# Kernel optimization log

Hardware: AMD Instinct MI355X
Metric: run time of the kernel (lower is better)

The kernel has to match this reference:

```python
import jax, jax.numpy as jnp
import numpy as np

P = 8          # patch_size
EPS = 1e-6     # LayerNorm2d eps


def _conv(x, w, b, groups=1):
    # x: (B,Cin,H,W), w: (Cout, Cin//groups, kh, kw)
    y = jax.lax.conv_general_dilated(
        x, w, window_strides=(1, 1), padding='SAME',
        feature_group_count=groups,
        dimension_numbers=('NCHW', 'OIHW', 'NCHW'))
    return y + b[None, :, None, None]


def _ln2d(x, w, b):
    mu = jnp.mean(x, axis=1, keepdims=True)
    var = jnp.mean((x - mu) ** 2, axis=1, keepdims=True)
    y = (x - mu) / jnp.sqrt(var + EPS)
    return w[None, :, None, None] * y + b[None, :, None, None]


def _fft_mix(x, fw):
    # windowed rFFT2 -> per-(channel,freq) real weight -> irFFT2.
    # H,W divisible by P, so window_partitionx == plain window partition.
    B, C, H, W = x.shape
    nh, nw = H // P, W // P
    xw = x.reshape(B, C, nh, P, nw, P).transpose(0, 2, 4, 1, 3, 5)  # (B,nh,nw,C,P,P)
    f = jnp.fft.rfft2(xw)                    # (B,nh,nw,C,P,P//2+1)
    f = f * fw                               # fw: (C,P,P//2+1) broadcasts
    xw = jnp.fft.irfft2(f, s=(P, P))
    return xw.transpose(0, 3, 1, 4, 2, 5).reshape(B, C, H, W)


def _gelu(x):
    return jax.nn.gelu(x, approximate=False)  # torch nn.GELU default = exact erf


def setup_inputs() -> dict:
    key = jax.random.key(0)
    ks = jax.random.split(key, 18)
    B, C, H, W = 4, 64, 256, 256
    C4, D = C * 4, C // 4
    f32 = jnp.float32

    def n(k, shape, s):
        return (jax.random.normal(k, shape, f32) * s)

    return {
        'x': jax.random.normal(ks[0], (B, C, H, W), f32),
        'ln_w': jnp.ones((C,), f32),
        'ln_b': jnp.zeros((C,), f32),
        'pconv_w': n(ks[1], (D, D, 3, 3), 0.08),
        'pconv_b': n(ks[2], (D,), 0.02),
        'w0': n(ks[3], (C4, C, 1, 1), 0.12),
        'b0': n(ks[4], (C4,), 0.02),
        'w1': n(ks[5], (C4, C, 1, 1), 0.12),
        'b1': n(ks[6], (C4,), 0.02),
        'w2': n(ks[7], (C, C4, 1, 1), 0.06),
        'b2': n(ks[8], (C,), 0.02),
        'w3': n(ks[9], (C4, 1, 3, 3), 0.3),
        'b3': n(ks[10], (C4,), 0.02),
        'w4': n(ks[11], (C, C4, 1, 1), 0.06),
        'b4': n(ks[12], (C,), 0.02),
        'fftw1': 1.0 + n(ks[13], (C, P, P // 2 + 1), 0.1),
        'fftw2': 1.0 + n(ks[14], (C, P, P // 2 + 1), 0.1),
    }


def reference(x, ln_w, ln_b, pconv_w, pconv_b, w0, b0, w1, b1,
              w2, b2, w3, b3, w4, b4, fftw1, fftw2):
    C = x.shape[1]
    D = C // 4
    C4 = C * 4

    xn = _ln2d(x, ln_w, ln_b)

    # partial 3x3 conv on first C//4 channels
    y1 = _conv(xn[:, :D], pconv_w, pconv_b)
    x2 = jnp.concatenate([y1, xn[:, D:]], axis=1)

    # branch 1: 1x1 expand -> GELU -> 1x1 contract -> windowed FFT mixing
    x1 = _conv(xn, w0, b0)
    x1 = _gelu(x1)
    x1 = _conv(x1, w2, b2)
    x1 = _fft_mix(x1, fftw1)

    # branch 2: 1x1 expand -> GELU -> depthwise 3x3 -> GELU -> 1x1 contract -> FFT mixing
    x2 = _conv(x2, w1, b1)
    x2 = _gelu(x2)
    x2 = _conv(x2, w3, b3, groups=C4)
    x2 = _gelu(x2)
    x2 = _conv(x2, w4, b4)
    x2 = _fft_mix(x2, fftw2)

    return x1 + x2
```

## Files before the change

### kernel.cpp

```cpp
#include <hip/hip_runtime.h>


typedef _Float16 f16;
typedef _Float16 f16x2 __attribute__((ext_vector_type(2)));
typedef _Float16 f16x4 __attribute__((ext_vector_type(4)));
typedef _Float16 f16x8 __attribute__((ext_vector_type(8)));
typedef float f32x4 __attribute__((ext_vector_type(4)));

__device__ __forceinline__ float dot2f(f16x2 a, f16x2 b, float c) {
#if __has_builtin(__builtin_amdgcn_fdot2)
  return __builtin_amdgcn_fdot2(a, b, c, false);
#else
  return c + (float)a.x * (float)b.x + (float)a.y * (float)b.y;
#endif
}

__device__ __forceinline__ f16x2 gelu_pk(f16x2 x) {
  const f16x2 c1 = {(f16)1.5957691f, (f16)1.5957691f};
  const f16x2 c3 = {(f16)0.0713548f, (f16)0.0713548f};
  const f16x2 cl = {(f16)-1.4426950f, (f16)-1.4426950f};
  f16x2 x2 = x * x;
  f16x2 u = x * (c1 + c3 * x2);
  f16x2 a = cl * u;
  f16 t0, t1;
#if __has_builtin(__builtin_amdgcn_exp2h)
  t0 = __builtin_amdgcn_exp2h(a[0]);
  t1 = __builtin_amdgcn_exp2h(a[1]);
#else
  t0 = (f16)exp2f((float)a[0]);
  t1 = (f16)exp2f((float)a[1]);
#endif
  f16 d0 = (f16)1.0f + t0, d1 = (f16)1.0f + t1;
  f16 r0, r1;
#if __has_builtin(__builtin_amdgcn_rcph)
  r0 = __builtin_amdgcn_rcph(d0);
  r1 = __builtin_amdgcn_rcph(d1);
#else
  r0 = (f16)(1.0f / (float)d0);
  r1 = (f16)(1.0f / (float)d1);
#endif
  f16x2 r = {r0, r1};
  return x * r;
}

__device__ __forceinline__ f16x2 cvtpk(float a, float b) {
  return __builtin_bit_cast(f16x2, __builtin_amdgcn_cvt_pkrtz(a, b));
}

__global__ void __launch_bounds__(256) lnpre_kernel(
    const float* __restrict__ x, const float* __restrict__ lnw,
    const float* __restrict__ lnb, f16* __restrict__ xn,
    const float* __restrict__ w0, const float* __restrict__ w1,
    const float* __restrict__ w2, const float* __restrict__ w4,
    const float* __restrict__ w3, const float* __restrict__ b3,
    const float* __restrict__ fw1, const float* __restrict__ fw2,
    f16* __restrict__ W0h, f16* __restrict__ W1h,
    f16* __restrict__ W2h, f16* __restrict__ W4h,
    f16* __restrict__ w3pk, f16* __restrict__ b3pk,
    float* __restrict__ kap1, float* __restrict__ kap2) {
  __shared__ float Wt[4][64];
  __shared__ float ct[8];
  int blk = blockIdx.x, t = threadIdx.x;
  if (blk < 1024) {
    int b = blk >> 8;
    int px = (blk & 255) * 256 + t;
    const float* xp = x + ((size_t)b << 22) + px;
    float v[64];
    float s = 0.f;
#pragma unroll
    for (int c = 0; c < 64; ++c) { v[c] = xp[(size_t)c << 16]; s += v[c]; }
    float mu = s * (1.f / 64.f), s2 = 0.f;
#pragma unroll
    for (int c = 0; c < 64; ++c) { float d = v[c] - mu; s2 += d * d; }
    float rstd = rsqrtf(s2 * (1.f / 64.f) + 1e-6f);
    f16* op = xn + (size_t)b * 4194304 + (size_t)px * 64;
#pragma unroll
    for (int g = 0; g < 8; ++g) {
      f16x8 pk;
#pragma unroll
      for (int j = 0; j < 8; ++j) {
        int c = g * 8 + j;
        pk[j] = (f16)((v[c] - mu) * rstd * lnw[c] + lnb[c]);
      }
      *(f16x8*)(op + g * 8) = pk;
    }
    return;
  }
  if (blk < 1290) {
    int i = (blk - 1024) * 256 + t;
    if (i < 16384) W0h[i] = (f16)w0[i];
    else if (i < 32768) W1h[i - 16384] = (f16)w1[i - 16384];
    else if (i < 49152) W2h[i - 32768] = (f16)w2[i - 32768];
    else if (i < 65536) W4h[i - 49152] = (f16)w4[i - 49152];
    else if (i < 67840) {
      int j = i - 65536;
      int g = j / 72, r = j % 72, tap = r >> 3, k = r & 7;
      w3pk[j] = (f16)w3[(g * 8 + k) * 9 + tap];
    } else if (i < 68096) {
      int k = i - 67840;
      b3pk[k] = (f16)b3[k];
    }
    return;
  }
  int sub = t >> 6, lane = t & 63;
  int unit = (blk - 1290) * 4 + sub;
  int which = unit >> 6, c = unit & 63;
  const float* fw = which ? fw2 : fw1;
  float* kap = which ? kap2 : kap1;
  int a = lane >> 3, bb = lane & 7;
  if (t == 0) {
    const float r2 = 0.70710678118654752440f;
    ct[0] = 1.f; ct[1] = r2; ct[2] = 0.f; ct[3] = -r2;
    ct[4] = -1.f; ct[5] = -r2; ct[6] = 0.f; ct[7] = r2;
  }
  Wt[sub][lane] = (bb <= 4) ? fw[c * 40 + a * 5 + bb]
                            : fw[c * 40 + ((8 - a) & 7) * 5 + (8 - bb)];
  __syncthreads();
  float acc = 0.f;
  for (int u = 0; u < 8; ++u)
    for (int v = 0; v < 8; ++v)
      acc += Wt[sub][u * 8 + v] * ct[(u * a + v * bb) & 7];
  kap[c * 64 + lane] = acc * 0.015625f;
}

__device__ __forceinline__ void pconv_body(
    char* smem, int blk, int b, const f16* __restrict__ xn,
    const float* __restrict__ pw, const float* __restrict__ pb,
    f16* __restrict__ y1) {
  char* halo = smem;
  f16* wpk = (f16*)(smem + 11520);
  float* pbs = (float*)(smem + 16128);
  int t = threadIdx.x;
  const f16* xnb = xn + (size_t)b * 4194304;
  f16* y1b = y1 + (size_t)b * 1048576;
  int h0 = (blk >> 4) << 4, w0 = (blk & 15) << 4;
  for (int i = t; i < 2304; i += 256) {
    int co = i / 144, r = i % 144, tap = r >> 4, ci = r & 15;
    wpk[i] = (f16)pw[co * 144 + ci * 9 + tap];
  }
  if (t < 16) pbs[t] = pb[t];
  for (int i = 0; i < 3; ++i) {
    int u = i * 256 + t;
    if (u < 648) {
      int hp = u >> 1, half = u & 1;
      int hr = hp / 18, hc = hp - hr * 18;
      int h = h0 - 1 + hr, w = w0 - 1 + hc;
      f16x8 v = {0, 0, 0, 0, 0, 0, 0, 0};
      if ((unsigned)h < 256u && (unsigned)w < 256u)
        v = *(const f16x8*)(xnb + ((((size_t)h << 8)) + w) * 64 + half * 8);
      *(f16x8*)(halo + hr * 640 + ((hc * 32 + half * 16) ^ ((hr & 7) << 4))) = v;
    }
  }
  __syncthreads();
  int rl = t >> 4, cl = t & 15;
  float acc[16];
#pragma unroll
  for (int co = 0; co < 16; ++co) acc[co] = pbs[co];
#pragma unroll
  for (int ty = 0; ty < 3; ++ty)
#pragma unroll
    for (int tx = 0; tx < 3; ++tx) {
      int hr = rl + ty, hc = cl + tx, tap = ty * 3 + tx;
      f16x8 ld0 = *(const f16x8*)(halo + hr * 640 + ((hc * 32) ^ ((hr & 7) << 4)));
      f16x8 ld1 = *(const f16x8*)(halo + hr * 640 + ((hc * 32 + 16) ^ ((hr & 7) << 4)));
#pragma unroll
      for (int co = 0; co < 16; ++co) {
#pragma unroll
        for (int p = 0; p < 4; ++p) {
          f16x2 xp = {ld0[2 * p], ld0[2 * p + 1]};
          f16x2 wp = *(const f16x2*)&wpk[co * 144 + tap * 16 + 2 * p];
          acc[co] = dot2f(xp, wp, acc[co]);
        }
#pragma unroll
        for (int p = 0; p < 4; ++p) {
          f16x2 xp = {ld1[2 * p], ld1[2 * p + 1]};
          f16x2 wp = *(const f16x2*)&wpk[co * 144 + tap * 16 + 8 + 2 * p];
          acc[co] = dot2f(xp, wp, acc[co]);
        }
      }
    }
  size_t px = (((size_t)(h0 + rl)) << 8) + w0 + cl;
  f16x8 o0, o1;
#pragma unroll
  for (int j = 0; j < 8; ++j) { o0[j] = (f16)acc[j]; o1[j] = (f16)acc[8 + j]; }
  *(f16x8*)(y1b + px * 16) = o0;
  *(f16x8*)(y1b + px * 16 + 8) = o1;
}

__device__ __forceinline__ void b1_body(
    char* smem, int sub, int b, const f16* __restrict__ xn,
    const f16* __restrict__ W0h, const float* __restrict__ b0,
    const f16* __restrict__ W2h, const float* __restrict__ b2,
    f16* __restrict__ u1d, f16* __restrict__ u1w) {
  f16* Es = (f16*)smem;
  int t = threadIdx.x;
  const f16* xnb = xn + (size_t)b * 4194304;
  f16* u1b = (b < 3) ? (u1d + (size_t)b * 4194304) : u1w;
  int px0 = sub << 7;
  int l = t & 63, wv = t >> 6, lm = l & 15, kg = l >> 4;
  f16x8 a[2][2];
#pragma unroll
  for (int mt = 0; mt < 2; ++mt) {
    int row = wv * 32 + mt * 16 + lm;
#pragma unroll
    for (int kk = 0; kk < 2; ++kk)
      a[mt][kk] = *(const f16x8*)(xnb + (size_t)(px0 + row) * 64 + kk * 32 + kg * 8);
  }
  f32x4 uacc[2][4];
#pragma unroll
  for (int aa = 0; aa < 2; ++aa)
#pragma unroll
    for (int n = 0; n < 4; ++n) uacc[aa][n] = (f32x4){0.f, 0.f, 0.f, 0.f};
  for (int cc = 0; cc < 4; ++cc) {
    f32x4 eacc[2][4];
#pragma unroll
    for (int aa = 0; aa < 2; ++aa)
#pragma unroll
      for (int n = 0; n < 4; ++n) eacc[aa][n] = (f32x4){0.f, 0.f, 0.f, 0.f};
#pragma unroll
    for (int kk = 0; kk < 2; ++kk) {
      f16x8 bf[4];
#pragma unroll
      for (int nt = 0; nt < 4; ++nt) {
        int co = cc * 64 + nt * 16 + lm;
        bf[nt] = *(const f16x8*)(W0h + (size_t)co * 64 + kk * 32 + kg * 8);
      }
#pragma unroll
      for (int mt = 0; mt < 2; ++mt)
#pragma unroll
        for (int nt = 0; nt < 4; ++nt)
          eacc[mt][nt] = __builtin_amdgcn_mfma_f32_16x16x32_f16(bf[nt], a[mt][kk], eacc[mt][nt], 0, 0, 0);
    }
    if (cc) __syncthreads();
#pragma unroll
    for (int mt = 0; mt < 2; ++mt) {
      int row = wv * 32 + mt * 16 + lm;
#pragma unroll
      for (int nt = 0; nt < 4; ++nt) {
        int c0 = nt * 16 + kg * 4;
        float4 bz4 = *(const float4*)&b0[cc * 64 + c0];
        f16x2 lo = gelu_pk(cvtpk(eacc[mt][nt][0] + bz4.x, eacc[mt][nt][1] + bz4.y));
        f16x2 hi = gelu_pk(cvtpk(eacc[mt][nt][2] + bz4.z, eacc[mt][nt][3] + bz4.w));
        f16x4 pk = {lo[0], lo[1], hi[0], hi[1]};
        *(f16x4*)((char*)Es + row * 128 + ((c0 * 2) ^ ((row & 7) << 4))) = pk;
      }
    }
    __syncthreads();
#pragma unroll
    for (int kk = 0; kk < 2; ++kk) {
      int kb = kk * 64 + kg * 16;
      f16x8 af[2];
#pragma unroll
      for (int mt = 0; mt < 2; ++mt) {
        int row = wv * 32 + mt * 16 + lm;
        af[mt] = *(const f16x8*)((char*)Es + row * 128 + (kb ^ ((row & 7) << 4)));
      }
      f16x8 bf[4];
#pragma unroll
      for (int nt = 0; nt < 4; ++nt) {
        int co = nt * 16 + lm;
        bf[nt] = *(const f16x8*)(W2h + (size_t)co * 256 + cc * 64 + kk * 32 + kg * 8);
      }
#pragma unroll
      for (int mt = 0; mt < 2; ++mt)
#pragma unroll
        for (int nt = 0; nt < 4; ++nt)
          uacc[mt][nt] = __builtin_amdgcn_mfma_f32_16x16x32_f16(bf[nt], af[mt], uacc[mt][nt], 0, 0, 0);
    }
    __syncthreads();
  }
#pragma unroll
  for (int mt = 0; mt < 2; ++mt) {
    int row = wv * 32 + mt * 16 + lm;
#pragma unroll
    for (int nt = 0; nt < 4; ++nt) {
      int c0 = nt * 16 + kg * 4;
      float4 bz4 = *(const float4*)&b2[c0];
      f16x2 lo = cvtpk(uacc[mt][nt][0] + bz4.x, uacc[mt][nt][1] + bz4.y);
      f16x2 hi = cvtpk(uacc[mt][nt][2] + bz4.z, uacc[mt][nt][3] + bz4.w);
      f16x4 pk = {lo[0], lo[1], hi[0], hi[1]};
      *(f16x4*)((char*)Es + row * 128 + ((c0 * 2) ^ ((row & 7) << 4))) = pk;
    }
  }
  __syncthreads();
  int co = t >> 2, q = t & 3;
  f16x8 o[4];
#pragma unroll
  for (int i = 0; i < 32; ++i) {
    int m = q * 32 + i;
    o[i >> 3][i & 7] =
        *(const f16*)((char*)Es + m * 128 + ((co * 2) ^ ((m & 7) << 4)));
  }
  f16* up = u1b + ((size_t)co << 16) + px0 + q * 32;
#pragma unroll
  for (int ss = 0; ss < 4; ++ss) *(f16x8*)(up + ss * 8) = o[ss];
}

__global__ void __launch_bounds__(256) b1pc_kernel(
    const f16* __restrict__ xn, const f16* __restrict__ W0h,
    const float* __restrict__ b0, const f16* __restrict__ W2h,
    const float* __restrict__ b2, f16* __restrict__ u1d,
    f16* __restrict__ u1w, const float* __restrict__ pw,
    const float* __restrict__ pb, f16* __restrict__ y1) {
  __shared__ __align__(16) char smem[16384];
  int xb = blockIdx.x;
  if (xb < 2048)
    b1_body(smem, xb & 511, xb >> 9, xn, W0h, b0, W2h, b2, u1d, u1w);
  else {
    int u = xb - 2048;
    pconv_body(smem, u & 255, u >> 8, xn, pw, pb, y1);
  }
}

__device__ __forceinline__ void b2_expand(
    const f16x8 (&a0)[3], const f16x8 (&a1)[3], const f16* __restrict__ W1h,
    int ce0, int lm, int kg, f32x4 (&eacc)[3][2]) {
#pragma unroll
  for (int a = 0; a < 3; ++a)
#pragma unroll
    for (int n = 0; n < 2; ++n) eacc[a][n] = (f32x4){0.f, 0.f, 0.f, 0.f};
#pragma unroll
  for (int kk = 0; kk < 2; ++kk) {
    f16x8 bf[2];
#pragma unroll
    for (int nt = 0; nt < 2; ++nt) {
      int ce = ce0 + nt * 16 + lm;
      bf[nt] = *(const f16x8*)(W1h + (size_t)ce * 64 + kk * 32 + kg * 8);
    }
#pragma unroll
    for (int mtl = 0; mtl < 3; ++mtl) {
      f16x8 af = kk ? a1[mtl] : a0[mtl];
#pragma unroll
      for (int nt = 0; nt < 2; ++nt)
        eacc[mtl][nt] = __builtin_amdgcn_mfma_f32_16x16x32_f16(bf[nt], af, eacc[mtl][nt], 0, 0, 0);
    }
  }
}

__global__ void __launch_bounds__(256) b2_kernel(
    const f16* __restrict__ xn, const f16* __restrict__ y1,
    const f16* __restrict__ W1h, const float* __restrict__ b1v,
    const f16* __restrict__ W4h, const float* __restrict__ b4,
    const f16* __restrict__ w3pk, const f16* __restrict__ b3pk,
    f16* __restrict__ u2) {
  __shared__ __align__(16) f16 Es[6144];
  int t = threadIdx.x, blk = blockIdx.x, b = blockIdx.y;
  const f16* xnb = xn + (size_t)b * 4194304;
  const f16* y1b = y1 + (size_t)b * 1048576;
  f16* u2b = u2 + (size_t)b * 4194304;
  int h0 = (blk >> 4) << 3, w0 = (blk & 15) << 4;
  int l = t & 63, wv = t >> 6, lm = l & 15, kg = l >> 4;
  f16x8 a0[3], a1[3];
#pragma unroll
  for (int mtl = 0; mtl < 3; ++mtl) {
    int row = (mtl * 4 + wv) * 16 + lm;
    f16x8 v0 = {0, 0, 0, 0, 0, 0, 0, 0}, v1 = v0;
    if (row < 180) {
      int hr = row / 18, hc = row - hr * 18;
      int h = h0 - 1 + hr, w = w0 - 1 + hc;
      if ((unsigned)h < 256u && (unsigned)w < 256u) {
        size_t px = ((size_t)h << 8) + w;
        v1 = *(const f16x8*)(xnb + px * 64 + 32 + kg * 8);
        v0 = (kg < 2) ? *(const f16x8*)(y1b + px * 16 + kg * 8)
                      : *(const f16x8*)(xnb + px * 64 + kg * 8);
      }
    }
    a0[mtl] = v0;
    a1[mtl] = v1;
  }
  f32x4 uacc[2][4];
#pragma unroll
  for (int a = 0; a < 2; ++a)
#pragma unroll
    for (int n = 0; n < 4; ++n) uacc[a][n] = (f32x4){0.f, 0.f, 0.f, 0.f};
  f32x4 eacc[3][2];
  b2_expand(a0, a1, W1h, 0, lm, kg, eacc);
  for (int it = 0; it < 8; ++it) {
    int ce0 = it * 32;
    if (it) __syncthreads();
#pragma unroll
    for (int mtl = 0; mtl < 3; ++mtl) {
      int row = (mtl * 4 + wv) * 16 + lm;
#pragma unroll
      for (int nt = 0; nt < 2; ++nt) {
        int cL = nt * 16 + kg * 4;
        float4 bz4 = *(const float4*)&b1v[ce0 + cL];
        f16x2 lo = gelu_pk(cvtpk(eacc[mtl][nt][0] + bz4.x, eacc[mtl][nt][1] + bz4.y));
        f16x2 hi = gelu_pk(cvtpk(eacc[mtl][nt][2] + bz4.z, eacc[mtl][nt][3] + bz4.w));
        f16x4 pk = {lo[0], lo[1], hi[0], hi[1]};
        *(f16x4*)((char*)Es + row * 64 + ((cL * 2) ^ (((row >> 1) & 3) << 4))) = pk;
      }
    }
    __syncthreads();
    if (it < 7) b2_expand(a0, a1, W1h, ce0 + 32, lm, kg, eacc);
    int g9 = (ce0 + kg * 8) >> 3;
    f16x8 wv9[9];
#pragma unroll
    for (int tap = 0; tap < 9; ++tap)
      wv9[tap] = *(const f16x8*)(w3pk + g9 * 72 + tap * 8);
    f16x8 bias8 = *(const f16x8*)(b3pk + ce0 + kg * 8);
    f16x8 af2[2];
#pragma unroll
    for (int mt = 0; mt < 2; ++mt) {
      int px = wv * 32 + mt * 16 + lm;
      int rl2 = px >> 4, cl2 = px & 15;
      f16x8 a8 = bias8;
#pragma unroll
      for (int ty = 0; ty < 3; ++ty)
#pragma unroll
        for (int tx = 0; tx < 3; ++tx) {
          int hp = (rl2 + ty) * 18 + (cl2 + tx);
          f16x8 xv = *(const f16x8*)((char*)Es + hp * 64 + ((kg * 16) ^ (((hp >> 1) & 3) << 4)));
          a8 += xv * wv9[ty * 3 + tx];
        }
#pragma unroll
      for (int j2 = 0; j2 < 4; ++j2) {
        f16x2 g = gelu_pk((f16x2){a8[2 * j2], a8[2 * j2 + 1]});
        af2[mt][2 * j2] = g[0];
        af2[mt][2 * j2 + 1] = g[1];
      }
    }
    f16x8 bf2[4];
#pragma unroll
    for (int nt = 0; nt < 4; ++nt) {
      int co = nt * 16 + lm;
      bf2[nt] = *(const f16x8*)(W4h + (size_t)co * 256 + ce0 + kg * 8);
    }
#pragma unroll
    for (int mt = 0; mt < 2; ++mt)
#pragma unroll
      for (int nt = 0; nt < 4; ++nt)
        uacc[mt][nt] = __builtin_amdgcn_mfma_f32_16x16x32_f16(bf2[nt], af2[mt], uacc[mt][nt], 0, 0, 0);
  }
  __syncthreads();
#pragma unroll
  for (int mt = 0; mt < 2; ++mt) {
    if (mt) __syncthreads();
    int crow = wv * 16 + lm;
#pragma unroll
    for (int nt = 0; nt < 4; ++nt) {
      int c0 = nt * 16 + kg * 4;
      float4 bz4 = *(const float4*)&b4[c0];
      f16x2 lo = cvtpk(uacc[mt][nt][0] + bz4.x, uacc[mt][nt][1] + bz4.y);
      f16x2 hi = cvtpk(uacc[mt][nt][2] + bz4.z, uacc[mt][nt][3] + bz4.w);
      f16x4 pk = {lo[0], lo[1], hi[0], hi[1]};
      *(f16x4*)((char*)Es + crow * 128 + ((c0 * 2) ^ ((crow & 7) << 4))) = pk;
    }
    __syncthreads();
    int co = t >> 2, q = t & 3;
    f16x8 o0, o1;
#pragma unroll
    for (int i = 0; i < 16; ++i) {
      int crow = q * 16 + i;
      f16 vv = *(const f16*)((char*)Es + crow * 128 + ((co * 2) ^ ((crow & 7) << 4)));
      if (i < 8) o0[i] = vv;
      else o1[i - 8] = vv;
    }
    f16* up = u2b + ((size_t)co << 16) + (size_t)(h0 + 2 * q + mt) * 256 + w0;
    *(f16x8*)(up) = o0;
    *(f16x8*)(up + 8) = o1;
  }
}

__global__ void __launch_bounds__(256) fftmix_kernel(
    const f16* __restrict__ u1d, const f16* __restrict__ u1w,
    const f16* __restrict__ u2, const float* __restrict__ kap1,
    const float* __restrict__ kap2, float* __restrict__ out, int base) {
  int blk = blockIdx.x;
  int b = base + blockIdx.y;
  int c = blk >> 4, part = blk & 15;
  int t = threadIdx.x;
  int l = t & 63, wv = (t >> 6) & 3;
  int s = l >> 3, tq = l & 7;
  __shared__ unsigned int kls[64];
  if (t < 64) {
    f16 k1 = (f16)kap1[(c << 6) + t];
    f16 k2 = (f16)kap2[(c << 6) + t];
    kls[t] = (unsigned int)__builtin_bit_cast(unsigned short, k1) |
             ((unsigned int)__builtin_bit_cast(unsigned short, k2) << 16);
  }
  __syncthreads();
  unsigned int kp[64];
#pragma unroll
  for (int j = 0; j < 64; ++j) {
    int idx = (((s - (j >> 3)) & 7) << 3) | ((tq - (j & 7)) & 7);
    kp[j] = kls[idx];
  }
  const f16* u1 = (b < 3) ? (u1d + (size_t)b * 4194304) : u1w;
  const f16* u2b = u2 + (size_t)b * 4194304;
  size_t cb = ((size_t)c) << 16;
  size_t obase = ((size_t)(b * 64 + c)) << 16;
  int win0 = part * 64 + wv * 16;
  for (int it = 0; it < 16; ++it) {
    int win = win0 + it;
    int wh = win >> 5, ww = win & 31;
    size_t pix = (size_t)((wh * 8 + s) << 8) + ww * 8 + tq;
    unsigned int pk =
        (unsigned int)__builtin_bit_cast(unsigned short, u1[cb + pix]) |
        ((unsigned int)__builtin_bit_cast(unsigned short, u2b[cb + pix]) << 16);
    float ac0 = 0.f, ac1 = 0.f, ac2 = 0.f, ac3 = 0.f;
#pragma unroll
    for (int j = 0; j < 64; j += 4) {
      unsigned int v0 = (unsigned int)__builtin_amdgcn_readlane((int)pk, j);
      unsigned int v1 = (unsigned int)__builtin_amdgcn_readlane((int)pk, j + 1);
      unsigned int v2 = (unsigned int)__builtin_amdgcn_readlane((int)pk, j + 2);
      unsigned int v3 = (unsigned int)__builtin_amdgcn_readlane((int)pk, j + 3);
      ac0 = dot2f(__builtin_bit_cast(f16x2, v0), __builtin_bit_cast(f16x2, kp[j]), ac0);
      ac1 = dot2f(__builtin_bit_cast(f16x2, v1), __builtin_bit_cast(f16x2, kp[j + 1]), ac1);
      ac2 = dot2f(__builtin_bit_cast(f16x2, v2), __builtin_bit_cast(f16x2, kp[j + 2]), ac2);
      ac3 = dot2f(__builtin_bit_cast(f16x2, v3), __builtin_bit_cast(f16x2, kp[j + 3]), ac3);
    }
    out[obase + pix] = (ac0 + ac1) + (ac2 + ac3);
  }
}

__global__ void diag_kernel(float* __restrict__ out, float code, int n) {
  int i = blockIdx.x * 256 + threadIdx.x;
  for (int p = i; p < n; p += 256 * 4096) out[p] = (p == 0) ? code : 0.f;
}

extern "C" void kernel_launch(void* const* d_in, const int* in_sizes, int n_in,
                              void* d_out, int out_size, void* d_ws,
                              size_t ws_size, hipStream_t stream) {
  const float* x       = (const float*)d_in[0];
  const float* ln_w    = (const float*)d_in[1];
  const float* ln_b    = (const float*)d_in[2];
  const float* pconv_w = (const float*)d_in[3];
  const float* pconv_b = (const float*)d_in[4];
  const float* w0      = (const float*)d_in[5];
  const float* b0      = (const float*)d_in[6];
  const float* w1      = (const float*)d_in[7];
  const float* b1      = (const float*)d_in[8];
  const float* w2      = (const float*)d_in[9];
  const float* b2      = (const float*)d_in[10];
  const float* w3      = (const float*)d_in[11];
  const float* b3      = (const float*)d_in[12];
  const float* w4      = (const float*)d_in[13];
  const float* b4      = (const float*)d_in[14];
  const float* fftw1   = (const float*)d_in[15];
  const float* fftw2   = (const float*)d_in[16];

  const size_t OFF_KAP1 = 0;
  const size_t OFF_KAP2 = 16384;
  const size_t OFF_W0H  = 32768;
  const size_t OFF_W1H  = 65536;
  const size_t OFF_W2H  = 98304;
  const size_t OFF_W4H  = 131072;
  const size_t OFF_W3PK = 163840;
  const size_t OFF_B3PK = 168448;
  const size_t OFF_Y1   = 168960;
  const size_t OFF_U2   = OFF_Y1 + 8388608ull;
  const size_t OFF_U13  = OFF_U2 + 33554432ull;
  const size_t WS_NEED  = OFF_U13 + 8388608ull;

  float* outF = (float*)d_out;
  if (ws_size < WS_NEED) {
    diag_kernel<<<4096, 256, 0, stream>>>(outF, 1000.0f + (float)(ws_size >> 20), 16777216);
    return;
  }
  char* ws = (char*)d_ws;
  float* kap1 = (float*)(ws + OFF_KAP1);
  float* kap2 = (float*)(ws + OFF_KAP2);
  f16* W0h  = (f16*)(ws + OFF_W0H);
  f16* W1h  = (f16*)(ws + OFF_W1H);
  f16* W2h  = (f16*)(ws + OFF_W2H);
  f16* W4h  = (f16*)(ws + OFF_W4H);
  f16* w3pk = (f16*)(ws + OFF_W3PK);
  f16* b3pk = (f16*)(ws + OFF_B3PK);
  f16* Y1   = (f16*)(ws + OFF_Y1);
  f16* U2   = (f16*)(ws + OFF_U2);
  f16* U13  = (f16*)(ws + OFF_U13);

  f16* XN  = (f16*)d_out;
  f16* U1D = (f16*)d_out + 16777216;

  lnpre_kernel<<<1322, 256, 0, stream>>>(x, ln_w, ln_b, XN,
                                         w0, w1, w2, w4, w3, b3, fftw1, fftw2,
                                         W0h, W1h, W2h, W4h, w3pk, b3pk,
                                         kap1, kap2);
  b1pc_kernel<<<3072, 256, 0, stream>>>(XN, W0h, b0, W2h, b2, U1D, U13,
                                        pconv_w, pconv_b, Y1);
  b2_kernel<<<dim3(512, 4), 256, 0, stream>>>(XN, Y1, W1h, b1, W4h, b4,
                                              w3pk, b3pk, U2);
  fftmix_kernel<<<dim3(1024, 2), 256, 0, stream>>>(U1D, U13, U2, kap1, kap2, outF, 0);
  fftmix_kernel<<<dim3(1024, 1), 256, 0, stream>>>(U1D, U13, U2, kap1, kap2, outF, 2);
  fftmix_kernel<<<dim3(1024, 1), 256, 0, stream>>>(U1D, U13, U2, kap1, kap2, outF, 3);
}
```

Baseline: 329.2 us.

## Double-buffer LDS staging in branch kernels and software-pipeline b1 expand

Both the b1 and b2 branch kernels now alternate between two LDS buffers across channel chunks, which removes one barrier per iteration. In b1 the next chunk's expand MFMAs are issued after the barrier so they can overlap with the contract stage, mirroring what b2 already did. The cost is double the shared memory per block (32KB and 24KB), which may lower occupancy, and higher register pressure from the extra live accumulators in b1.

```diff
diff --git a/kernel.cpp b/kernel.cpp
--- a/kernel.cpp
+++ b/kernel.cpp
@@ -187,12 +187,34 @@
   *(f16x8*)(y1b + px * 16 + 8) = o1;
 }
 
+__device__ __forceinline__ void b1_expand(
+    const f16x8 (&a)[2][2], const f16* __restrict__ W0h, int cc, int lm,
+    int kg, f32x4 (&eacc)[2][4]) {
+#pragma unroll
+  for (int aa = 0; aa < 2; ++aa)
+#pragma unroll
+    for (int n = 0; n < 4; ++n) eacc[aa][n] = (f32x4){0.f, 0.f, 0.f, 0.f};
+#pragma unroll
+  for (int kk = 0; kk < 2; ++kk) {
+    f16x8 bf[4];
+#pragma unroll
+    for (int nt = 0; nt < 4; ++nt) {
+      int co = cc * 64 + nt * 16 + lm;
+      bf[nt] = *(const f16x8*)(W0h + (size_t)co * 64 + kk * 32 + kg * 8);
+    }
+#pragma unroll
+    for (int mt = 0; mt < 2; ++mt)
+#pragma unroll
+      for (int nt = 0; nt < 4; ++nt)
+        eacc[mt][nt] = __builtin_amdgcn_mfma_f32_16x16x32_f16(bf[nt], a[mt][kk], eacc[mt][nt], 0, 0, 0);
+  }
+}
+
 __device__ __forceinline__ void b1_body(
     char* smem, int sub, int b, const f16* __restrict__ xn,
     const f16* __restrict__ W0h, const float* __restrict__ b0,
     const f16* __restrict__ W2h, const float* __restrict__ b2,
     f16* __restrict__ u1d, f16* __restrict__ u1w) {
-  f16* Es = (f16*)smem;
   int t = threadIdx.x;
   const f16* xnb = xn + (size_t)b * 4194304;
   f16* u1b = (b < 3) ? (u1d + (size_t)b * 4194304) : u1w;
@@ -211,27 +233,10 @@
   for (int aa = 0; aa < 2; ++aa)
 #pragma unroll
     for (int n = 0; n < 4; ++n) uacc[aa][n] = (f32x4){0.f, 0.f, 0.f, 0.f};
+  f32x4 eacc[2][4];
+  b1_expand(a, W0h, 0, lm, kg, eacc);
   for (int cc = 0; cc < 4; ++cc) {
-    f32x4 eacc[2][4];
-#pragma unroll
-    for (int aa = 0; aa < 2; ++aa)
-#pragma unroll
-      for (int n = 0; n < 4; ++n) eacc[aa][n] = (f32x4){0.f, 0.f, 0.f, 0.f};
-#pragma unroll
-    for (int kk = 0; kk < 2; ++kk) {
-      f16x8 bf[4];
-#pragma unroll
-      for (int nt = 0; nt < 4; ++nt) {
-        int co = cc * 64 + nt * 16 + lm;
-        bf[nt] = *(const f16x8*)(W0h + (size_t)co * 64 + kk * 32 + kg * 8);
-      }
-#pragma unroll
-      for (int mt = 0; mt < 2; ++mt)
-#pragma unroll
-        for (int nt = 0; nt < 4; ++nt)
-          eacc[mt][nt] = __builtin_amdgcn_mfma_f32_16x16x32_f16(bf[nt], a[mt][kk], eacc[mt][nt], 0, 0, 0);
-    }
-    if (cc) __syncthreads();
+    char* Es = smem + ((cc & 1) << 14);
 #pragma unroll
     for (int mt = 0; mt < 2; ++mt) {
       int row = wv * 32 + mt * 16 + lm;
@@ -242,10 +247,11 @@
         f16x2 lo = gelu_pk(cvtpk(eacc[mt][nt][0] + bz4.x, eacc[mt][nt][1] + bz4.y));
         f16x2 hi = gelu_pk(cvtpk(eacc[mt][nt][2] + bz4.z, eacc[mt][nt][3] + bz4.w));
         f16x4 pk = {lo[0], lo[1], hi[0], hi[1]};
-        *(f16x4*)((char*)Es + row * 128 + ((c0 * 2) ^ ((row & 7) << 4))) = pk;
+        *(f16x4*)(Es + row * 128 + ((c0 * 2) ^ ((row & 7) << 4))) = pk;
       }
     }
     __syncthreads();
+    if (cc < 3) b1_expand(a, W0h, cc + 1, lm, kg, eacc);
 #pragma unroll
     for (int kk = 0; kk < 2; ++kk) {
       int kb = kk * 64 + kg * 16;
@@ -253,7 +259,7 @@
 #pragma unroll
       for (int mt = 0; mt < 2; ++mt) {
         int row = wv * 32 + mt * 16 + lm;
-        af[mt] = *(const f16x8*)((char*)Es + row * 128 + (kb ^ ((row & 7) << 4)));
+        af[mt] = *(const f16x8*)(Es + row * 128 + (kb ^ ((row & 7) << 4)));
       }
       f16x8 bf[4];
 #pragma unroll
@@ -267,8 +273,9 @@
         for (int nt = 0; nt < 4; ++nt)
           uacc[mt][nt] = __builtin_amdgcn_mfma_f32_16x16x32_f16(bf[nt], af[mt], uacc[mt][nt], 0, 0, 0);
     }
-    __syncthreads();
-  }
+  }
+  __syncthreads();
+  char* Es = smem;
 #pragma unroll
   for (int mt = 0; mt < 2; ++mt) {
     int row = wv * 32 + mt * 16 + lm;
@@ -279,7 +286,7 @@
       f16x2 lo = cvtpk(uacc[mt][nt][0] + bz4.x, uacc[mt][nt][1] + bz4.y);
       f16x2 hi = cvtpk(uacc[mt][nt][2] + bz4.z, uacc[mt][nt][3] + bz4.w);
       f16x4 pk = {lo[0], lo[1], hi[0], hi[1]};
-      *(f16x4*)((char*)Es + row * 128 + ((c0 * 2) ^ ((row & 7) << 4))) = pk;
+      *(f16x4*)(Es + row * 128 + ((c0 * 2) ^ ((row & 7) << 4))) = pk;
     }
   }
   __syncthreads();
@@ -288,8 +295,7 @@
 #pragma unroll
   for (int i = 0; i < 32; ++i) {
     int m = q * 32 + i;
-    o[i >> 3][i & 7] =
-        *(const f16*)((char*)Es + m * 128 + ((co * 2) ^ ((m & 7) << 4)));
+    o[i >> 3][i & 7] = *(const f16*)(Es + m * 128 + ((co * 2) ^ ((m & 7) << 4)));
   }
   f16* up = u1b + ((size_t)co << 16) + px0 + q * 32;
 #pragma unroll
@@ -302,7 +308,7 @@
     const float* __restrict__ b2, f16* __restrict__ u1d,
     f16* __restrict__ u1w, const float* __restrict__ pw,
     const float* __restrict__ pb, f16* __restrict__ y1) {
-  __shared__ __align__(16) char smem[16384];
+  __shared__ __align__(16) char smem[32768];
   int xb = blockIdx.x;
   if (xb < 2048)
     b1_body(smem, xb & 511, xb >> 9, xn, W0h, b0, W2h, b2, u1d, u1w);
@@ -343,7 +349,7 @@
     const f16* __restrict__ W4h, const float* __restrict__ b4,
     const f16* __restrict__ w3pk, const f16* __restrict__ b3pk,
     f16* __restrict__ u2) {
-  __shared__ __align__(16) f16 Es[6144];
+  __shared__ __align__(16) char EsBuf[24576];
   int t = threadIdx.x, blk = blockIdx.x, b = blockIdx.y;
   const f16* xnb = xn + (size_t)b * 4194304;
   const f16* y1b = y1 + (size_t)b * 1048576;
@@ -377,7 +383,7 @@
   b2_expand(a0, a1, W1h, 0, lm, kg, eacc);
   for (int it = 0; it < 8; ++it) {
     int ce0 = it * 32;
-    if (it) __syncthreads();
+    char* Es = EsBuf + ((it & 1) * 12288);
 #pragma unroll
     for (int mtl = 0; mtl < 3; ++mtl) {
       int row = (mtl * 4 + wv) * 16 + lm;
@@ -388,7 +394,7 @@
         f16x2 lo = gelu_pk(cvtpk(eacc[mtl][nt][0] + bz4.x, eacc[mtl][nt][1] + bz4.y));
         f16x2 hi = gelu_pk(cvtpk(eacc[mtl][nt][2] + bz4.z, eacc[mtl][nt][3] + bz4.w));
         f16x4 pk = {lo[0], lo[1], hi[0], hi[1]};
-        *(f16x4*)((char*)Es + row * 64 + ((cL * 2) ^ (((row >> 1) & 3) << 4))) = pk;
+        *(f16x4*)(Es + row * 64 + ((cL * 2) ^ (((row >> 1) & 3) << 4))) = pk;
       }
     }
     __syncthreads();
@@ -410,7 +416,7 @@
 #pragma unroll
         for (int tx = 0; tx < 3; ++tx) {
           int hp = (rl2 + ty) * 18 + (cl2 + tx);
-          f16x8 xv = *(const f16x8*)((char*)Es + hp * 64 + ((kg * 16) ^ (((hp >> 1) & 3) << 4)));
+          f16x8 xv = *(const f16x8*)(Es + hp * 64 + ((kg * 16) ^ (((hp >> 1) & 3) << 4)));
           a8 += xv * wv9[ty * 3 + tx];
         }
 #pragma unroll
@@ -433,6 +439,7 @@
         uacc[mt][nt] = __builtin_amdgcn_mfma_f32_16x16x32_f16(bf2[nt], af2[mt], uacc[mt][nt], 0, 0, 0);
   }
   __syncthreads();
+  char* Ep = EsBuf;
 #pragma unroll
   for (int mt = 0; mt < 2; ++mt) {
     if (mt) __syncthreads();
@@ -444,7 +451,7 @@
       f16x2 lo = cvtpk(uacc[mt][nt][0] + bz4.x, uacc[mt][nt][1] + bz4.y);
       f16x2 hi = cvtpk(uacc[mt][nt][2] + bz4.z, uacc[mt][nt][3] + bz4.w);
       f16x4 pk = {lo[0], lo[1], hi[0], hi[1]};
-      *(f16x4*)((char*)Es + crow * 128 + ((c0 * 2) ^ ((crow & 7) << 4))) = pk;
+      *(f16x4*)(Ep + crow * 128 + ((c0 * 2) ^ ((crow & 7) << 4))) = pk;
     }
     __syncthreads();
     int co = t >> 2, q = t & 3;
@@ -452,7 +459,7 @@
 #pragma unroll
     for (int i = 0; i < 16; ++i) {
       int crow = q * 16 + i;
-      f16 vv = *(const f16*)((char*)Es + crow * 128 + ((co * 2) ^ ((crow & 7) << 4)));
+      f16 vv = *(const f16*)(Ep + crow * 128 + ((co * 2) ^ ((crow & 7) << 4)));
       if (i < 8) o0[i] = vv;
       else o1[i - 8] = vv;
     }
```

After: 344.9 us. 4.8% more time.
